# Optimization experiments

Measured on AMD Instinct MI355X. Metric: run time of the kernel, lower is better.

Reference implementation:

```python
import jax, jax.numpy as jnp
import numpy as np

NEG_INF = -1e9

def setup_inputs() -> dict:
    key = jax.random.key(0)
    ks = jax.random.split(key, 8)
    B, Np1, D, k = 16, 10001, 128, 16
    return {
        "query": jax.random.normal(ks[0], (B, D), jnp.float32),
        "psi_prime": jax.random.normal(ks[1], (B, Np1, D), jnp.float32),
        "knn_indices": jax.random.randint(ks[2], (B, Np1, k), 0, Np1, jnp.int64),
        "mask": jnp.zeros((B, Np1), dtype=bool),
        "current_coords": jax.random.uniform(ks[3], (B, 2), jnp.float32),
        "all_coords": jax.random.uniform(ks[4], (B, Np1, 2), jnp.float32),
        "demands": jax.random.uniform(ks[5], (B, Np1), jnp.float32),
        "lambda_param": jnp.float32(0.1),
        "mu_param": jnp.float32(0.5),
        "nu_param": jnp.float32(0.0),
    }

def _eknn(psi_prime, knn_indices):
    # psi_prime: [B, N+1, D], knn_indices: [B, N+1, k] -> interference [B, N+1]
    B, Np1, k = knn_indices.shape
    D = psi_prime.shape[-1]
    flat_idx = knn_indices.reshape(B, Np1 * k, 1)  # gather along node axis
    neighbors = jnp.take_along_axis(psi_prime, flat_idx, axis=1).reshape(B, Np1, k, D)
    return jnp.einsum("bnd,bnkd->bn", psi_prime, neighbors)

def reference(query, psi_prime, knn_indices, mask, current_coords, all_coords,
              demands, lambda_param, mu_param, nu_param):
    capacity = 1.0  # default forward arg
    context_scores = jnp.einsum("bnd,bd->bn", psi_prime, query)
    interference = _eknn(psi_prime, knn_indices)
    dist_to_nodes = jnp.linalg.norm(all_coords - current_coords[:, None, :], axis=-1)
    mu_eff = jnp.clip(mu_param, 0.0, 20.0)
    lam_eff = jnp.clip(lambda_param, -2.0, 3.0)
    nu_eff = jnp.clip(nu_param, -2.0, 3.0)
    scores = context_scores + lam_eff * interference - mu_eff * dist_to_nodes
    cap_val = max(float(capacity), 1e-8)
    scores = scores + nu_eff * (demands / cap_val)
    scores = jnp.where(mask, NEG_INF, scores)
    return jax.nn.log_softmax(scores, axis=-1)
```

## Files before the change

### kernel.cpp

```cpp
#include <hip/hip_runtime.h>
#include <math.h>

#define BATCH 16
#define NP1   10001
#define KNN   16
#define DIM   128
#define NEG_INF_F (-1e9f)
#define TOTAL_NODES ((long)BATCH * NP1)
#define SLAB_BYTES  ((size_t)BATCH * NP1 * DIM)
#define NXCD 8
#define EXP_OFF 60.0f
#define NBUCK 64

typedef __attribute__((ext_vector_type(2))) float f32x2;

template <int SEL>
__device__ inline float f8tof(unsigned u) {
#if __has_builtin(__builtin_amdgcn_cvt_f32_fp8)
    return __builtin_amdgcn_cvt_f32_fp8((int)u, SEL);
#else
    const unsigned x = (u >> (8 * SEL)) & 0xFFu;
    const unsigned bits = ((x & 0x80u) << 24) | (((x & 0x7Fu) << 20) + 0x3C000000u);
    return (x & 0x7Fu) ? __uint_as_float(bits) : 0.f;
#endif
}

__device__ inline f32x2 pk2lo(unsigned u) {
#if __has_builtin(__builtin_amdgcn_cvt_pk_f32_fp8)
    return __builtin_amdgcn_cvt_pk_f32_fp8((int)u, false);
#else
    f32x2 r; r.x = f8tof<0>(u); r.y = f8tof<1>(u); return r;
#endif
}
__device__ inline f32x2 pk2hi(unsigned u) {
#if __has_builtin(__builtin_amdgcn_cvt_pk_f32_fp8)
    return __builtin_amdgcn_cvt_pk_f32_fp8((int)u, true);
#else
    f32x2 r; r.x = f8tof<2>(u); r.y = f8tof<3>(u); return r;
#endif
}

#if !__has_builtin(__builtin_amdgcn_cvt_pk_fp8_f32)
__device__ inline unsigned enc1_fp8(float f) {
    const unsigned u = __float_as_uint(f);
    const unsigned s = (u >> 31) << 7;
    unsigned v = u + 0x80000u;
    int e8 = (int)((v >> 23) & 0xFFu) - 120;
    if (e8 <= 0) return s;
    if (e8 > 15) { e8 = 15; v |= 0x700000u; }
    return s | ((unsigned)e8 << 3) | ((v >> 20) & 7u);
}
#endif

__device__ inline unsigned pk_fp8x4(float4 v) {
#if __has_builtin(__builtin_amdgcn_cvt_pk_fp8_f32)
    int w = __builtin_amdgcn_cvt_pk_fp8_f32(v.x, v.y, 0, false);
    w = __builtin_amdgcn_cvt_pk_fp8_f32(v.z, v.w, w, true);
    return (unsigned)w;
#else
    return enc1_fp8(v.x) | (enc1_fp8(v.y) << 8) | (enc1_fp8(v.z) << 16) | (enc1_fp8(v.w) << 24);
#endif
}

__device__ inline unsigned xcd_chunk_swizzle(unsigned b, unsigned nwg) {
    const unsigned xcd = b % NXCD, i = b / NXCD;
    const unsigned q = nwg / NXCD, r = nwg % NXCD;
    const unsigned base = (xcd < r) ? xcd * (q + 1) : r * (q + 1) + (xcd - r) * q;
    return base + i;
}

__global__ __launch_bounds__(256) void hs_prep_kernel(
    const float* __restrict__ query, const float* __restrict__ psi,
    const float* __restrict__ cur, const float* __restrict__ coords,
    const float* __restrict__ demands, const float* __restrict__ mu_p,
    const float* __restrict__ nu_p, unsigned* __restrict__ slab,
    float* __restrict__ out, float* __restrict__ bucket)
{
    if (blockIdx.x == 0) {
#pragma unroll
        for (int i = 0; i < (BATCH * NBUCK) / 256; ++i)
            bucket[threadIdx.x + i * 256] = 0.f;
    }
    const unsigned lb = xcd_chunk_swizzle(blockIdx.x, gridDim.x);
    const long row = (long)lb * 8 + (threadIdx.x >> 5);
    if (row >= TOTAL_NODES) return;
    const int l32 = threadIdx.x & 31;
    const int b = (int)(row / NP1);

    const float4 v = ((const float4*)psi)[row * 32 + l32];
    const float4 q = ((const float4*)query)[(long)b * 32 + l32];

    slab[row * 32 + l32] = pk_fp8x4(v);

    float ctx = v.x * q.x + v.y * q.y + v.z * q.z + v.w * q.w;
#pragma unroll
    for (int off = 16; off > 0; off >>= 1) ctx += __shfl_xor(ctx, off, 64);

    if (l32 == 0) {
        const float mu = fminf(fmaxf(mu_p[0], 0.f), 20.f);
        const float nu = fminf(fmaxf(nu_p[0], -2.f), 3.f);
        const float dx = coords[row * 2 + 0] - cur[b * 2 + 0];
        const float dy = coords[row * 2 + 1] - cur[b * 2 + 1];
        out[row] = ctx - mu * sqrtf(dx * dx + dy * dy) + nu * demands[row];
    }
}

__global__ __launch_bounds__(256) void hs_gather_kernel(
    const int* __restrict__ knn,
    const unsigned char* __restrict__ mask,
    const uint4* __restrict__ slab4,
    const float* __restrict__ lam_p,
    float* __restrict__ out,
    float* __restrict__ bucket)
{
    __shared__ float s_val[16];
    __shared__ int   s_bat[16];

    const unsigned lb = xcd_chunk_swizzle(blockIdx.x, gridDim.x);
    const int wid  = threadIdx.x >> 6;
    const int lane = threadIdx.x & 63;
    const int qw   = lane >> 4;
    const int l16  = lane & 15;
    const int j8   = l16 & 7;
    const int h    = l16 >> 3;
    const long node = ((long)lb * 4 + wid) * 4 + qw;
    const int b = (int)(node / NP1);
    const uint4* gb = slab4 + (long)b * NP1 * 8;

    float base = 0.f; int mk = 0;
    if (l16 == 0) { base = out[node]; mk = mask[node]; }

    const uint4 p = slab4[node * 8 + j8];
    const f32x2 p01 = pk2lo(p.x), p23 = pk2hi(p.x);
    const f32x2 p45 = pk2lo(p.y), p67 = pk2hi(p.y);
    const f32x2 p89 = pk2lo(p.z), pAB = pk2hi(p.z);
    const f32x2 pCD = pk2lo(p.w), pEF = pk2hi(p.w);

    const int4* kp = (const int4*)(knn + node * KNN);
    const int4 k0 = kp[0], k1 = kp[1], k2 = kp[2], k3 = kp[3];
    int idx[8];
    idx[0] = h ? k0.y : k0.x;
    idx[1] = h ? k0.w : k0.z;
    idx[2] = h ? k1.y : k1.x;
    idx[3] = h ? k1.w : k1.z;
    idx[4] = h ? k2.y : k2.x;
    idx[5] = h ? k2.w : k2.z;
    idx[6] = h ? k3.y : k3.x;
    idx[7] = h ? k3.w : k3.z;

    uint4 nb[8];
#pragma unroll
    for (int t = 0; t < 8; ++t) nb[t] = gb[(long)idx[t] * 8 + j8];

    float a0 = 0.f, a1 = 0.f, a2 = 0.f, a3 = 0.f;
    float a4 = 0.f, a5 = 0.f, a6 = 0.f, a7 = 0.f;
#pragma unroll
    for (int t = 0; t < 8; ++t) {
        f32x2 c;
        c = pk2lo(nb[t].x); a0 = fmaf(c.x, p01.x, a0); a1 = fmaf(c.y, p01.y, a1);
        c = pk2hi(nb[t].x); a2 = fmaf(c.x, p23.x, a2); a3 = fmaf(c.y, p23.y, a3);
        c = pk2lo(nb[t].y); a4 = fmaf(c.x, p45.x, a4); a5 = fmaf(c.y, p45.y, a5);
        c = pk2hi(nb[t].y); a6 = fmaf(c.x, p67.x, a6); a7 = fmaf(c.y, p67.y, a7);
        c = pk2lo(nb[t].z); a0 = fmaf(c.x, p89.x, a0); a1 = fmaf(c.y, p89.y, a1);
        c = pk2hi(nb[t].z); a2 = fmaf(c.x, pAB.x, a2); a3 = fmaf(c.y, pAB.y, a3);
        c = pk2lo(nb[t].w); a4 = fmaf(c.x, pCD.x, a4); a5 = fmaf(c.y, pCD.y, a5);
        c = pk2hi(nb[t].w); a6 = fmaf(c.x, pEF.x, a6); a7 = fmaf(c.y, pEF.y, a7);
    }
    float interf = ((a0 + a1) + (a2 + a3)) + ((a4 + a5) + (a6 + a7));

#pragma unroll
    for (int off = 8; off > 0; off >>= 1) interf += __shfl_xor(interf, off, 64);

    const int slot = wid * 4 + qw;
    if (l16 == 0) {
        const float lam = fminf(fmaxf(lam_p[0], -2.f), 3.f);
        float s = base + lam * interf;
        if (mk) s = NEG_INF_F;
        out[node] = s;
        s_val[slot] = expf(s - EXP_OFF);
        s_bat[slot] = b;
    }
    __syncthreads();

    if (threadIdx.x == 0) {
        float sum0 = 0.f, sum1 = 0.f;
        const int b0 = s_bat[0];
        int b1 = -1;
#pragma unroll
        for (int i = 0; i < 16; ++i) {
            if (s_bat[i] == b0) sum0 += s_val[i];
            else { b1 = s_bat[i]; sum1 += s_val[i]; }
        }
        const int bk = blockIdx.x & (NBUCK - 1);
        atomicAdd(&bucket[b0 * NBUCK + bk], sum0);
        if (b1 >= 0) atomicAdd(&bucket[b1 * NBUCK + bk], sum1);
    }
}

__global__ __launch_bounds__(256) void hs_finalize_kernel(
    float* __restrict__ out, const float* __restrict__ bucket)
{
    __shared__ float s_part[256];
    __shared__ float s_lse[BATCH];

    {
        const int t = threadIdx.x;
        const int bb = t >> 4, j = t & 15;
        s_part[t] = bucket[bb * NBUCK + j] + bucket[bb * NBUCK + j + 16]
                  + bucket[bb * NBUCK + j + 32] + bucket[bb * NBUCK + j + 48];
    }
    __syncthreads();
    if (threadIdx.x < BATCH) {
        float s = 0.f;
#pragma unroll
        for (int i = 0; i < 16; ++i) s += s_part[threadIdx.x * 16 + i];
        s_lse[threadIdx.x] = EXP_OFF + logf(s);
    }
    __syncthreads();

    const long t = (long)blockIdx.x * blockDim.x + threadIdx.x;
    const long n4 = TOTAL_NODES / 4;
    if (t >= n4) return;
    float4 v = ((float4*)out)[t];
    const long e0 = t * 4;
    v.x -= s_lse[(int)((e0    ) / NP1)];
    v.y -= s_lse[(int)((e0 + 1) / NP1)];
    v.z -= s_lse[(int)((e0 + 2) / NP1)];
    v.w -= s_lse[(int)((e0 + 3) / NP1)];
    ((float4*)out)[t] = v;
}

__global__ __launch_bounds__(256) void hs_scores_f32_kernel(
    const float* __restrict__ query, const float* __restrict__ psi,
    const int* __restrict__ knn, const unsigned char* __restrict__ mask,
    const float* __restrict__ cur, const float* __restrict__ coords,
    const float* __restrict__ demands, const float* __restrict__ lam_p,
    const float* __restrict__ mu_p, const float* __restrict__ nu_p,
    float* __restrict__ out)
{
    const int wid  = threadIdx.x >> 6;
    const int lane = threadIdx.x & 63;
    const int half = lane >> 5;
    const int l32  = lane & 31;
    const long node = (long)blockIdx.x * 4 + wid;
    if (node >= TOTAL_NODES) return;
    const int b = (int)(node / NP1);

    const float4* psi4 = (const float4*)psi;
    const float4* gb   = psi4 + (long)b * NP1 * 32;

    const float4 p = psi4[node * 32 + l32];
    const float4 q = ((const float4*)query)[(long)b * 32 + l32];
    float ctx = p.x * q.x + p.y * q.y + p.z * q.z + p.w * q.w;

    const int2* kp2 = (const int2*)(knn + node * KNN);
    int idxs[KNN / 2];
#pragma unroll
    for (int t = 0; t < KNN / 2; ++t) {
        const int2 pr = kp2[t];
        idxs[t] = half ? pr.y : pr.x;
    }
    float4 nb[KNN / 2];
#pragma unroll
    for (int t = 0; t < KNN / 2; ++t) nb[t] = gb[(long)idxs[t] * 32 + l32];

    float4 s0;
    s0.x = ((nb[0].x + nb[1].x) + (nb[2].x + nb[3].x)) + ((nb[4].x + nb[5].x) + (nb[6].x + nb[7].x));
    s0.y = ((nb[0].y + nb[1].y) + (nb[2].y + nb[3].y)) + ((nb[4].y + nb[5].y) + (nb[6].y + nb[7].y));
    s0.z = ((nb[0].z + nb[1].z) + (nb[2].z + nb[3].z)) + ((nb[4].z + nb[5].z) + (nb[6].z + nb[7].z));
    s0.w = ((nb[0].w + nb[1].w) + (nb[2].w + nb[3].w)) + ((nb[4].w + nb[5].w) + (nb[6].w + nb[7].w));
    float interf = p.x * s0.x + p.y * s0.y + p.z * s0.z + p.w * s0.w;

#pragma unroll
    for (int off = 32; off > 0; off >>= 1) {
        ctx    += __shfl_xor(ctx, off, 64);
        interf += __shfl_xor(interf, off, 64);
    }
    if (lane == 0) {
        const float lam = fminf(fmaxf(lam_p[0], -2.f), 3.f);
        const float mu  = fminf(fmaxf(mu_p[0],   0.f), 20.f);
        const float nu  = fminf(fmaxf(nu_p[0],  -2.f), 3.f);
        const float dx = coords[node * 2 + 0] - cur[b * 2 + 0];
        const float dy = coords[node * 2 + 1] - cur[b * 2 + 1];
        float s = 0.5f * ctx + lam * interf - mu * sqrtf(dx * dx + dy * dy) + nu * demands[node];
        if (mask[node]) s = NEG_INF_F;
        out[node] = s;
    }
}

#define LSM_T 1024
__global__ __launch_bounds__(LSM_T) void hs_lsm_kernel(float* __restrict__ out)
{
    const int b = blockIdx.x;
    float* row = out + (long)b * NP1;
    const int lane = threadIdx.x & 63;
    const int wid  = threadIdx.x >> 6;
    __shared__ float red[LSM_T / 64];

    float v[10];
    float mx = -INFINITY;
#pragma unroll
    for (int i = 0; i < 10; ++i) {
        const int idx = threadIdx.x + i * LSM_T;
        v[i] = (idx < NP1) ? row[idx] : -INFINITY;
        mx = fmaxf(mx, v[i]);
    }
#pragma unroll
    for (int off = 32; off > 0; off >>= 1) mx = fmaxf(mx, __shfl_xor(mx, off, 64));
    if (lane == 0) red[wid] = mx;
    __syncthreads();
    if (wid == 0) {
        float m = (lane < LSM_T / 64) ? red[lane] : -INFINITY;
#pragma unroll
        for (int off = 8; off > 0; off >>= 1) m = fmaxf(m, __shfl_xor(m, off, 64));
        if (lane == 0) red[0] = m;
    }
    __syncthreads();
    mx = red[0];
    __syncthreads();

    float sum = 0.f;
#pragma unroll
    for (int i = 0; i < 10; ++i) {
        const int idx = threadIdx.x + i * LSM_T;
        if (idx < NP1) sum += expf(v[i] - mx);
    }
#pragma unroll
    for (int off = 32; off > 0; off >>= 1) sum += __shfl_xor(sum, off, 64);
    if (lane == 0) red[wid] = sum;
    __syncthreads();
    if (wid == 0) {
        float s = (lane < LSM_T / 64) ? red[lane] : 0.f;
#pragma unroll
        for (int off = 8; off > 0; off >>= 1) s += __shfl_xor(s, off, 64);
        if (lane == 0) red[0] = s;
    }
    __syncthreads();
    const float lse = mx + logf(red[0]);
#pragma unroll
    for (int i = 0; i < 10; ++i) {
        const int idx = threadIdx.x + i * LSM_T;
        if (idx < NP1) row[idx] = v[i] - lse;
    }
}

extern "C" void kernel_launch(void* const* d_in, const int* in_sizes, int n_in,
                              void* d_out, int out_size, void* d_ws, size_t ws_size,
                              hipStream_t stream) {
    (void)in_sizes; (void)n_in; (void)out_size;

    const float* query   = (const float*)d_in[0];
    const float* psi     = (const float*)d_in[1];
    const int*   knn     = (const int*)d_in[2];
    const unsigned char* mask = (const unsigned char*)d_in[3];
    const float* cur     = (const float*)d_in[4];
    const float* coords  = (const float*)d_in[5];
    const float* demands = (const float*)d_in[6];
    const float* lam_p   = (const float*)d_in[7];
    const float* mu_p    = (const float*)d_in[8];
    const float* nu_p    = (const float*)d_in[9];
    float* out = (float*)d_out;

    const size_t bucket_bytes = (size_t)BATCH * NBUCK * sizeof(float);

    if (ws_size >= SLAB_BYTES + bucket_bytes) {
        unsigned* slab = (unsigned*)d_ws;
        float* bucket  = (float*)((char*)d_ws + SLAB_BYTES);

        const int prep_blocks = (int)((TOTAL_NODES + 7) / 8);
        hipLaunchKernelGGL(hs_prep_kernel, dim3(prep_blocks), dim3(256), 0, stream,
                           query, psi, cur, coords, demands, mu_p, nu_p, slab, out,
                           bucket);

        const int gat_blocks = (int)(TOTAL_NODES / 16);
        hipLaunchKernelGGL(hs_gather_kernel, dim3(gat_blocks), dim3(256), 0, stream,
                           knn, mask, (const uint4*)d_ws, lam_p, out, bucket);

        const int fin_blocks = (int)((TOTAL_NODES / 4 + 255) / 256);
        hipLaunchKernelGGL(hs_finalize_kernel, dim3(fin_blocks), dim3(256), 0, stream,
                           out, bucket);
    } else {
        const int blocks = (int)((TOTAL_NODES + 3) / 4);
        hipLaunchKernelGGL(hs_scores_f32_kernel, dim3(blocks), dim3(256), 0, stream,
                           query, psi, knn, mask, cur, coords, demands,
                           lam_p, mu_p, nu_p, out);
        hipLaunchKernelGGL(hs_lsm_kernel, dim3(BATCH), dim3(LSM_T), 0, stream, out);
    }
}
```

Before: 58.54 us.

## Split batch in halves to overlap gather of first half with prep of second

Prep and gather are now split by batch halves, giving three launches: prep of batches 0-7, a combined kernel that gathers batches 0-7 while prepping batches 8-15, and a final gather of batches 8-15. Overlapping the bandwidth-heavy prep with the latency-bound gather is meant to hide the idle phase between the kernels. Block-to-node mapping now interleaves the eight batches by blockIdx low bits instead of the XCD chunk swizzle, so each block handles a single batch and needs only one atomic. The cost is an extra launch and possible contention between the two kinds of work inside the mid kernel.

```diff
diff --git a/kernel.cpp b/kernel.cpp
--- a/kernel.cpp
+++ b/kernel.cpp
@@ -8,9 +8,12 @@
 #define NEG_INF_F (-1e9f)
 #define TOTAL_NODES ((long)BATCH * NP1)
 #define SLAB_BYTES  ((size_t)BATCH * NP1 * DIM)
-#define NXCD 8
 #define EXP_OFF 60.0f
 #define NBUCK 64
+
+#define PREP_HALF_BLOCKS 10008
+#define GAT_HALF_BLOCKS  5008
+#define MID_BLOCKS (GAT_HALF_BLOCKS + PREP_HALF_BLOCKS)
 
 typedef __attribute__((ext_vector_type(2))) float f32x2;
 
@@ -24,7 +27,6 @@
     return (x & 0x7Fu) ? __uint_as_float(bits) : 0.f;
 #endif
 }
-
 __device__ inline f32x2 pk2lo(unsigned u) {
 #if __has_builtin(__builtin_amdgcn_cvt_pk_f32_fp8)
     return __builtin_amdgcn_cvt_pk_f32_fp8((int)u, false);
@@ -39,7 +41,6 @@
     f32x2 r; r.x = f8tof<2>(u); r.y = f8tof<3>(u); return r;
 #endif
 }
-
 #if !__has_builtin(__builtin_amdgcn_cvt_pk_fp8_f32)
 __device__ inline unsigned enc1_fp8(float f) {
     const unsigned u = __float_as_uint(f);
@@ -51,7 +52,6 @@
     return s | ((unsigned)e8 << 3) | ((v >> 20) & 7u);
 }
 #endif
-
 __device__ inline unsigned pk_fp8x4(float4 v) {
 #if __has_builtin(__builtin_amdgcn_cvt_pk_fp8_f32)
     int w = __builtin_amdgcn_cvt_pk_fp8_f32(v.x, v.y, 0, false);
@@ -62,14 +62,124 @@
 #endif
 }
 
-__device__ inline unsigned xcd_chunk_swizzle(unsigned b, unsigned nwg) {
-    const unsigned xcd = b % NXCD, i = b / NXCD;
-    const unsigned q = nwg / NXCD, r = nwg % NXCD;
-    const unsigned base = (xcd < r) ? xcd * (q + 1) : r * (q + 1) + (xcd - r) * q;
-    return base + i;
-}
-
-__global__ __launch_bounds__(256) void hs_prep_kernel(
+__device__ inline void prep_work(
+    int idx, int tid, int batch_base,
+    const float* __restrict__ query, const float* __restrict__ psi,
+    const float* __restrict__ cur, const float* __restrict__ coords,
+    const float* __restrict__ demands, const float* __restrict__ mu_p,
+    const float* __restrict__ nu_p, unsigned* __restrict__ slab,
+    float* __restrict__ out)
+{
+    const int bb  = batch_base + (idx & 7);
+    const int sub = idx >> 3;
+    const int hw  = tid >> 5;
+    const int l32 = tid & 31;
+    const int r   = sub * 8 + hw;
+    if (r >= NP1) return;
+    const long row = (long)bb * NP1 + r;
+
+    const float4 v = ((const float4*)psi)[row * 32 + l32];
+    const float4 q = ((const float4*)query)[(long)bb * 32 + l32];
+
+    slab[row * 32 + l32] = pk_fp8x4(v);
+
+    float ctx = v.x * q.x + v.y * q.y + v.z * q.z + v.w * q.w;
+#pragma unroll
+    for (int off = 16; off > 0; off >>= 1) ctx += __shfl_xor(ctx, off, 64);
+
+    if (l32 == 0) {
+        const float mu = fminf(fmaxf(mu_p[0], 0.f), 20.f);
+        const float nu = fminf(fmaxf(nu_p[0], -2.f), 3.f);
+        const float dx = coords[row * 2 + 0] - cur[bb * 2 + 0];
+        const float dy = coords[row * 2 + 1] - cur[bb * 2 + 1];
+        out[row] = ctx - mu * sqrtf(dx * dx + dy * dy) + nu * demands[row];
+    }
+}
+
+__device__ inline void gather_work(
+    int g, int tid, int batch_base,
+    const int* __restrict__ knn, const unsigned char* __restrict__ mask,
+    const uint4* __restrict__ slab4, const float* __restrict__ lam_p,
+    float* __restrict__ out, float* __restrict__ bucket, float* s_val)
+{
+    const int bb  = batch_base + (g & 7);
+    const int sub = g >> 3;
+    const int wid = tid >> 6, lane = tid & 63;
+    const int qw  = lane >> 4, l16 = lane & 15;
+    const int j8  = l16 & 7;
+    const int h   = l16 >> 3;
+    const int nloc = sub * 16 + wid * 4 + qw;
+    const bool valid = nloc < NP1;
+
+    float sval = 0.f;
+    if (valid) {
+        const long node = (long)bb * NP1 + nloc;
+        const uint4* gb = slab4 + (long)bb * NP1 * 8;
+
+        float base = 0.f; int mk = 0;
+        if (l16 == 0) { base = out[node]; mk = mask[node]; }
+
+        const uint4 p = slab4[node * 8 + j8];
+        const f32x2 p01 = pk2lo(p.x), p23 = pk2hi(p.x);
+        const f32x2 p45 = pk2lo(p.y), p67 = pk2hi(p.y);
+        const f32x2 p89 = pk2lo(p.z), pAB = pk2hi(p.z);
+        const f32x2 pCD = pk2lo(p.w), pEF = pk2hi(p.w);
+
+        const int4* kp = (const int4*)(knn + node * KNN);
+        const int4 k0 = kp[0], k1 = kp[1], k2 = kp[2], k3 = kp[3];
+        int idx[8];
+        idx[0] = h ? k0.y : k0.x;
+        idx[1] = h ? k0.w : k0.z;
+        idx[2] = h ? k1.y : k1.x;
+        idx[3] = h ? k1.w : k1.z;
+        idx[4] = h ? k2.y : k2.x;
+        idx[5] = h ? k2.w : k2.z;
+        idx[6] = h ? k3.y : k3.x;
+        idx[7] = h ? k3.w : k3.z;
+
+        uint4 nb[8];
+#pragma unroll
+        for (int t = 0; t < 8; ++t) nb[t] = gb[(long)idx[t] * 8 + j8];
+
+        float a0 = 0.f, a1 = 0.f, a2 = 0.f, a3 = 0.f;
+        float a4 = 0.f, a5 = 0.f, a6 = 0.f, a7 = 0.f;
+#pragma unroll
+        for (int t = 0; t < 8; ++t) {
+            f32x2 c;
+            c = pk2lo(nb[t].x); a0 = fmaf(c.x, p01.x, a0); a1 = fmaf(c.y, p01.y, a1);
+            c = pk2hi(nb[t].x); a2 = fmaf(c.x, p23.x, a2); a3 = fmaf(c.y, p23.y, a3);
+            c = pk2lo(nb[t].y); a4 = fmaf(c.x, p45.x, a4); a5 = fmaf(c.y, p45.y, a5);
+            c = pk2hi(nb[t].y); a6 = fmaf(c.x, p67.x, a6); a7 = fmaf(c.y, p67.y, a7);
+            c = pk2lo(nb[t].z); a0 = fmaf(c.x, p89.x, a0); a1 = fmaf(c.y, p89.y, a1);
+            c = pk2hi(nb[t].z); a2 = fmaf(c.x, pAB.x, a2); a3 = fmaf(c.y, pAB.y, a3);
+            c = pk2lo(nb[t].w); a4 = fmaf(c.x, pCD.x, a4); a5 = fmaf(c.y, pCD.y, a5);
+            c = pk2hi(nb[t].w); a6 = fmaf(c.x, pEF.x, a6); a7 = fmaf(c.y, pEF.y, a7);
+        }
+        float interf = ((a0 + a1) + (a2 + a3)) + ((a4 + a5) + (a6 + a7));
+#pragma unroll
+        for (int off = 8; off > 0; off >>= 1) interf += __shfl_xor(interf, off, 64);
+
+        if (l16 == 0) {
+            const float lam = fminf(fmaxf(lam_p[0], -2.f), 3.f);
+            float s = base + lam * interf;
+            if (mk) s = NEG_INF_F;
+            out[node] = s;
+            sval = expf(s - EXP_OFF);
+        }
+    }
+
+    const int slot = wid * 4 + qw;
+    if (l16 == 0) s_val[slot] = sval;
+    __syncthreads();
+    if (tid == 0) {
+        float sum = 0.f;
+#pragma unroll
+        for (int i = 0; i < 16; ++i) sum += s_val[i];
+        atomicAdd(&bucket[bb * NBUCK + (g & (NBUCK - 1))], sum);
+    }
+}
+
+__global__ __launch_bounds__(256) void hs_prep1_kernel(
     const float* __restrict__ query, const float* __restrict__ psi,
     const float* __restrict__ cur, const float* __restrict__ coords,
     const float* __restrict__ demands, const float* __restrict__ mu_p,
@@ -81,120 +191,37 @@
         for (int i = 0; i < (BATCH * NBUCK) / 256; ++i)
             bucket[threadIdx.x + i * 256] = 0.f;
     }
-    const unsigned lb = xcd_chunk_swizzle(blockIdx.x, gridDim.x);
-    const long row = (long)lb * 8 + (threadIdx.x >> 5);
-    if (row >= TOTAL_NODES) return;
-    const int l32 = threadIdx.x & 31;
-    const int b = (int)(row / NP1);
-
-    const float4 v = ((const float4*)psi)[row * 32 + l32];
-    const float4 q = ((const float4*)query)[(long)b * 32 + l32];
-
-    slab[row * 32 + l32] = pk_fp8x4(v);
-
-    float ctx = v.x * q.x + v.y * q.y + v.z * q.z + v.w * q.w;
-#pragma unroll
-    for (int off = 16; off > 0; off >>= 1) ctx += __shfl_xor(ctx, off, 64);
-
-    if (l32 == 0) {
-        const float mu = fminf(fmaxf(mu_p[0], 0.f), 20.f);
-        const float nu = fminf(fmaxf(nu_p[0], -2.f), 3.f);
-        const float dx = coords[row * 2 + 0] - cur[b * 2 + 0];
-        const float dy = coords[row * 2 + 1] - cur[b * 2 + 1];
-        out[row] = ctx - mu * sqrtf(dx * dx + dy * dy) + nu * demands[row];
-    }
-}
-
-__global__ __launch_bounds__(256) void hs_gather_kernel(
-    const int* __restrict__ knn,
-    const unsigned char* __restrict__ mask,
-    const uint4* __restrict__ slab4,
-    const float* __restrict__ lam_p,
-    float* __restrict__ out,
+    prep_work(blockIdx.x, threadIdx.x, 0, query, psi, cur, coords, demands,
+              mu_p, nu_p, slab, out);
+}
+
+__global__ __launch_bounds__(256) void hs_mid_kernel(
+    const float* __restrict__ query, const float* __restrict__ psi,
+    const float* __restrict__ cur, const float* __restrict__ coords,
+    const float* __restrict__ demands, const float* __restrict__ mu_p,
+    const float* __restrict__ nu_p, const float* __restrict__ lam_p,
+    const int* __restrict__ knn, const unsigned char* __restrict__ mask,
+    unsigned* __restrict__ slab, float* __restrict__ out,
     float* __restrict__ bucket)
 {
     __shared__ float s_val[16];
-    __shared__ int   s_bat[16];
-
-    const unsigned lb = xcd_chunk_swizzle(blockIdx.x, gridDim.x);
-    const int wid  = threadIdx.x >> 6;
-    const int lane = threadIdx.x & 63;
-    const int qw   = lane >> 4;
-    const int l16  = lane & 15;
-    const int j8   = l16 & 7;
-    const int h    = l16 >> 3;
-    const long node = ((long)lb * 4 + wid) * 4 + qw;
-    const int b = (int)(node / NP1);
-    const uint4* gb = slab4 + (long)b * NP1 * 8;
-
-    float base = 0.f; int mk = 0;
-    if (l16 == 0) { base = out[node]; mk = mask[node]; }
-
-    const uint4 p = slab4[node * 8 + j8];
-    const f32x2 p01 = pk2lo(p.x), p23 = pk2hi(p.x);
-    const f32x2 p45 = pk2lo(p.y), p67 = pk2hi(p.y);
-    const f32x2 p89 = pk2lo(p.z), pAB = pk2hi(p.z);
-    const f32x2 pCD = pk2lo(p.w), pEF = pk2hi(p.w);
-
-    const int4* kp = (const int4*)(knn + node * KNN);
-    const int4 k0 = kp[0], k1 = kp[1], k2 = kp[2], k3 = kp[3];
-    int idx[8];
-    idx[0] = h ? k0.y : k0.x;
-    idx[1] = h ? k0.w : k0.z;
-    idx[2] = h ? k1.y : k1.x;
-    idx[3] = h ? k1.w : k1.z;
-    idx[4] = h ? k2.y : k2.x;
-    idx[5] = h ? k2.w : k2.z;
-    idx[6] = h ? k3.y : k3.x;
-    idx[7] = h ? k3.w : k3.z;
-
-    uint4 nb[8];
-#pragma unroll
-    for (int t = 0; t < 8; ++t) nb[t] = gb[(long)idx[t] * 8 + j8];
-
-    float a0 = 0.f, a1 = 0.f, a2 = 0.f, a3 = 0.f;
-    float a4 = 0.f, a5 = 0.f, a6 = 0.f, a7 = 0.f;
-#pragma unroll
-    for (int t = 0; t < 8; ++t) {
-        f32x2 c;
-        c = pk2lo(nb[t].x); a0 = fmaf(c.x, p01.x, a0); a1 = fmaf(c.y, p01.y, a1);
-        c = pk2hi(nb[t].x); a2 = fmaf(c.x, p23.x, a2); a3 = fmaf(c.y, p23.y, a3);
-        c = pk2lo(nb[t].y); a4 = fmaf(c.x, p45.x, a4); a5 = fmaf(c.y, p45.y, a5);
-        c = pk2hi(nb[t].y); a6 = fmaf(c.x, p67.x, a6); a7 = fmaf(c.y, p67.y, a7);
-        c = pk2lo(nb[t].z); a0 = fmaf(c.x, p89.x, a0); a1 = fmaf(c.y, p89.y, a1);
-        c = pk2hi(nb[t].z); a2 = fmaf(c.x, pAB.x, a2); a3 = fmaf(c.y, pAB.y, a3);
-        c = pk2lo(nb[t].w); a4 = fmaf(c.x, pCD.x, a4); a5 = fmaf(c.y, pCD.y, a5);
-        c = pk2hi(nb[t].w); a6 = fmaf(c.x, pEF.x, a6); a7 = fmaf(c.y, pEF.y, a7);
-    }
-    float interf = ((a0 + a1) + (a2 + a3)) + ((a4 + a5) + (a6 + a7));
-
-#pragma unroll
-    for (int off = 8; off > 0; off >>= 1) interf += __shfl_xor(interf, off, 64);
-
-    const int slot = wid * 4 + qw;
-    if (l16 == 0) {
-        const float lam = fminf(fmaxf(lam_p[0], -2.f), 3.f);
-        float s = base + lam * interf;
-        if (mk) s = NEG_INF_F;
-        out[node] = s;
-        s_val[slot] = expf(s - EXP_OFF);
-        s_bat[slot] = b;
-    }
-    __syncthreads();
-
-    if (threadIdx.x == 0) {
-        float sum0 = 0.f, sum1 = 0.f;
-        const int b0 = s_bat[0];
-        int b1 = -1;
-#pragma unroll
-        for (int i = 0; i < 16; ++i) {
-            if (s_bat[i] == b0) sum0 += s_val[i];
-            else { b1 = s_bat[i]; sum1 += s_val[i]; }
-        }
-        const int bk = blockIdx.x & (NBUCK - 1);
-        atomicAdd(&bucket[b0 * NBUCK + bk], sum0);
-        if (b1 >= 0) atomicAdd(&bucket[b1 * NBUCK + bk], sum1);
-    }
+    if (blockIdx.x < GAT_HALF_BLOCKS) {
+        gather_work(blockIdx.x, threadIdx.x, 0, knn, mask,
+                    (const uint4*)slab, lam_p, out, bucket, s_val);
+    } else {
+        prep_work(blockIdx.x - GAT_HALF_BLOCKS, threadIdx.x, 8,
+                  query, psi, cur, coords, demands, mu_p, nu_p, slab, out);
+    }
+}
+
+__global__ __launch_bounds__(256) void hs_gat2_kernel(
+    const int* __restrict__ knn, const unsigned char* __restrict__ mask,
+    const uint4* __restrict__ slab4, const float* __restrict__ lam_p,
+    float* __restrict__ out, float* __restrict__ bucket)
+{
+    __shared__ float s_val[16];
+    gather_work(blockIdx.x, threadIdx.x, 8, knn, mask, slab4, lam_p, out,
+                bucket, s_val);
 }
 
 __global__ __launch_bounds__(256) void hs_finalize_kernel(
@@ -202,7 +229,6 @@
 {
     __shared__ float s_part[256];
     __shared__ float s_lse[BATCH];
-
     {
         const int t = threadIdx.x;
         const int bb = t >> 4, j = t & 15;
@@ -217,7 +243,6 @@
         s_lse[threadIdx.x] = EXP_OFF + logf(s);
     }
     __syncthreads();
-
     const long t = (long)blockIdx.x * blockDim.x + threadIdx.x;
     const long n4 = TOTAL_NODES / 4;
     if (t >= n4) return;
@@ -367,15 +392,13 @@
         unsigned* slab = (unsigned*)d_ws;
         float* bucket  = (float*)((char*)d_ws + SLAB_BYTES);
 
-        const int prep_blocks = (int)((TOTAL_NODES + 7) / 8);
-        hipLaunchKernelGGL(hs_prep_kernel, dim3(prep_blocks), dim3(256), 0, stream,
-                           query, psi, cur, coords, demands, mu_p, nu_p, slab, out,
-                           bucket);
-
-        const int gat_blocks = (int)(TOTAL_NODES / 16);
-        hipLaunchKernelGGL(hs_gather_kernel, dim3(gat_blocks), dim3(256), 0, stream,
+        hipLaunchKernelGGL(hs_prep1_kernel, dim3(PREP_HALF_BLOCKS), dim3(256), 0, stream,
+                           query, psi, cur, coords, demands, mu_p, nu_p, slab, out, bucket);
+        hipLaunchKernelGGL(hs_mid_kernel, dim3(MID_BLOCKS), dim3(256), 0, stream,
+                           query, psi, cur, coords, demands, mu_p, nu_p, lam_p,
+                           knn, mask, slab, out, bucket);
+        hipLaunchKernelGGL(hs_gat2_kernel, dim3(GAT_HALF_BLOCKS), dim3(256), 0, stream,
                            knn, mask, (const uint4*)d_ws, lam_p, out, bucket);
-
         const int fin_blocks = (int)((TOTAL_NODES / 4 + 255) / 256);
         hipLaunchKernelGGL(hs_finalize_kernel, dim3(fin_blocks), dim3(256), 0, stream,
                            out, bucket);
```

After: 60.39 us. 3.2% more time.
